# Kernel optimization log

Measured on AMD Instinct MI355X. Metric: run time of the kernel, lower is better.

Reference implementation:

```python
import jax, jax.numpy as jnp
import numpy as np

B, D, N_LAYER = 16384, 1024, 4  # cross_layer=3 -> n_layer=4
BN_EPS = 1e-5


def setup_inputs() -> dict:
    key = jax.random.key(0)
    kx, kw, kb = jax.random.split(key, 3)
    x = jax.random.normal(kx, (B, D), dtype=jnp.float32)
    weight_w = jax.random.normal(kw, (N_LAYER, D), dtype=jnp.float32)
    weight_b = jax.random.normal(kb, (N_LAYER, D), dtype=jnp.float32)
    return {"x": x, "weight_w": weight_w, "weight_b": weight_b}


def reference(x, weight_w, weight_b):
    # Per layer: res = BN(res + x0 * (res . w_l) + b_l)
    # (x0 res^T) @ w == x0 * (res . w): avoids the (B,D,D) outer product.
    x0 = x
    res = x
    for i in range(weight_w.shape[0]):
        s = res @ weight_w[i]                      # (B,) dot per row
        res = res + x0 * s[:, None] + weight_b[i]  # (B,D)
        mu = jnp.mean(res, axis=0)                 # BatchNorm1d, affine=False, train mode
        var = jnp.var(res, axis=0)                 # biased variance
        res = (res - mu) * jax.lax.rsqrt(var + BN_EPS)
    return res
```

## Files before the change

kernel.cpp:

```cpp
#include <hip/hip_runtime.h>


#define BB 16384
#define DD 1024
#define NL 4
#define BN_EPS 1e-5f

constexpr int ABLK = 1024;
constexpr int ROWS_PER_BLK = BB / ABLK;
constexpr int NB1 = 64;
constexpr int RED0 = ABLK / NB1;

template <bool FIRST>
__global__ __launch_bounds__(256) void layer_kernel(
    const float* __restrict__ x0,
    const float* Rin,
    float*       Rout,
    const float* __restrict__ w,
    const float* __restrict__ bias,
    const float* __restrict__ scale,
    const float* __restrict__ shift,
    float* __restrict__ Psum,
    float* __restrict__ Psq)
{
    __shared__ float red[2][2][4];
    const int tid  = threadIdx.x;
    const int lane = tid & 63;
    const int wv   = tid >> 6;
    const int c    = tid << 2;

    const float4 w4 = *(const float4*)(w + c);
    const float4 b4 = *(const float4*)(bias + c);
    float4 sc4, sh4;
    if (FIRST) {
        sc4 = make_float4(1.f, 1.f, 1.f, 1.f);
        sh4 = make_float4(0.f, 0.f, 0.f, 0.f);
    } else {
        sc4 = *(const float4*)(scale + c);
        sh4 = *(const float4*)(shift + c);
    }

    float4 asum = make_float4(0.f, 0.f, 0.f, 0.f);
    float4 asq  = make_float4(0.f, 0.f, 0.f, 0.f);

    const int r0 = blockIdx.x * ROWS_PER_BLK;

    for (int it = 0; it < ROWS_PER_BLK / 2; ++it) {
        const int r = r0 + it * 2;
        const size_t base0 = (size_t)r * DD + c;
        const size_t base1 = base0 + DD;

        float4 v0 = *(const float4*)(Rin + base0);
        float4 v1 = *(const float4*)(Rin + base1);
        float4 xv0, xv1;
        if (!FIRST) {
            xv0 = *(const float4*)(x0 + base0);
            xv1 = *(const float4*)(x0 + base1);
        }

        v0.x = fmaf(v0.x, sc4.x, sh4.x); v0.y = fmaf(v0.y, sc4.y, sh4.y);
        v0.z = fmaf(v0.z, sc4.z, sh4.z); v0.w = fmaf(v0.w, sc4.w, sh4.w);
        v1.x = fmaf(v1.x, sc4.x, sh4.x); v1.y = fmaf(v1.y, sc4.y, sh4.y);
        v1.z = fmaf(v1.z, sc4.z, sh4.z); v1.w = fmaf(v1.w, sc4.w, sh4.w);
        if (FIRST) { xv0 = v0; xv1 = v1; }

        float p0 = v0.x * w4.x + v0.y * w4.y + v0.z * w4.z + v0.w * w4.w;
        float p1 = v1.x * w4.x + v1.y * w4.y + v1.z * w4.z + v1.w * w4.w;

        #pragma unroll
        for (int off = 32; off; off >>= 1) {
            p0 += __shfl_down(p0, off, 64);
            p1 += __shfl_down(p1, off, 64);
        }
        const int slot = it & 1;
        if (lane == 0) { red[slot][0][wv] = p0; red[slot][1][wv] = p1; }
        __syncthreads();
        const float s0 = red[slot][0][0] + red[slot][0][1] +
                         red[slot][0][2] + red[slot][0][3];
        const float s1 = red[slot][1][0] + red[slot][1][1] +
                         red[slot][1][2] + red[slot][1][3];

        float4 n0, n1;
        n0.x = fmaf(xv0.x, s0, v0.x) + b4.x;
        n0.y = fmaf(xv0.y, s0, v0.y) + b4.y;
        n0.z = fmaf(xv0.z, s0, v0.z) + b4.z;
        n0.w = fmaf(xv0.w, s0, v0.w) + b4.w;
        n1.x = fmaf(xv1.x, s1, v1.x) + b4.x;
        n1.y = fmaf(xv1.y, s1, v1.y) + b4.y;
        n1.z = fmaf(xv1.z, s1, v1.z) + b4.z;
        n1.w = fmaf(xv1.w, s1, v1.w) + b4.w;

        *(float4*)(Rout + base0) = n0;
        *(float4*)(Rout + base1) = n1;

        asum.x += n0.x + n1.x; asum.y += n0.y + n1.y;
        asum.z += n0.z + n1.z; asum.w += n0.w + n1.w;
        asq.x = fmaf(n0.x, n0.x, asq.x); asq.x = fmaf(n1.x, n1.x, asq.x);
        asq.y = fmaf(n0.y, n0.y, asq.y); asq.y = fmaf(n1.y, n1.y, asq.y);
        asq.z = fmaf(n0.z, n0.z, asq.z); asq.z = fmaf(n1.z, n1.z, asq.z);
        asq.w = fmaf(n0.w, n0.w, asq.w); asq.w = fmaf(n1.w, n1.w, asq.w);
    }

    *(float4*)(Psum + (size_t)blockIdx.x * DD + c) = asum;
    *(float4*)(Psq  + (size_t)blockIdx.x * DD + c) = asq;
}

__global__ __launch_bounds__(256) void reduce0_kernel(
    const float* __restrict__ Psum, const float* __restrict__ Psq,
    float* __restrict__ Qsum, float* __restrict__ Qsq)
{
    const int c = threadIdx.x << 2;
    const int j = blockIdx.x;
    float4 a = make_float4(0.f, 0.f, 0.f, 0.f);
    float4 q = make_float4(0.f, 0.f, 0.f, 0.f);
    #pragma unroll
    for (int k = 0; k < RED0; ++k) {
        const size_t off = (size_t)(j * RED0 + k) * DD + c;
        const float4 ps = *(const float4*)(Psum + off);
        const float4 pq = *(const float4*)(Psq + off);
        a.x += ps.x; a.y += ps.y; a.z += ps.z; a.w += ps.w;
        q.x += pq.x; q.y += pq.y; q.z += pq.z; q.w += pq.w;
    }
    *(float4*)(Qsum + (size_t)j * DD + c) = a;
    *(float4*)(Qsq  + (size_t)j * DD + c) = q;
}

__global__ __launch_bounds__(256) void stats_kernel(
    const float* __restrict__ Qsum, const float* __restrict__ Qsq,
    float* __restrict__ scale, float* __restrict__ shift)
{
    const int d = blockIdx.x * 256 + threadIdx.x;
    float s = 0.f, q = 0.f;
    #pragma unroll 8
    for (int k = 0; k < NB1; ++k) {
        s += Qsum[k * DD + d];
        q += Qsq[k * DD + d];
    }
    const float mu  = s * (1.0f / BB);
    const float var = q * (1.0f / BB) - mu * mu;
    const float inv = rsqrtf(var + BN_EPS);
    scale[d] = inv;
    shift[d] = -mu * inv;
}

__global__ __launch_bounds__(256) void finalize_kernel(
    float* __restrict__ R,
    const float* __restrict__ scale, const float* __restrict__ shift)
{
    const size_t total = (size_t)BB * DD / 4;
    const size_t stride = (size_t)gridDim.x * blockDim.x;
    for (size_t i = (size_t)blockIdx.x * blockDim.x + threadIdx.x;
         i < total; i += stride) {
        const int c = (int)(i & (DD / 4 - 1)) << 2;
        float4 v = ((const float4*)R)[i];
        const float4 sc = *(const float4*)(scale + c);
        const float4 sh = *(const float4*)(shift + c);
        v.x = fmaf(v.x, sc.x, sh.x);
        v.y = fmaf(v.y, sc.y, sh.y);
        v.z = fmaf(v.z, sc.z, sh.z);
        v.w = fmaf(v.w, sc.w, sh.w);
        ((float4*)R)[i] = v;
    }
}

extern "C" void kernel_launch(void* const* d_in, const int* in_sizes, int n_in,
                              void* d_out, int out_size, void* d_ws, size_t ws_size,
                              hipStream_t stream) {
    const float* x  = (const float*)d_in[0];
    const float* ww = (const float*)d_in[1];
    const float* wb = (const float*)d_in[2];
    float* out = (float*)d_out;
    float* ws  = (float*)d_ws;

    float* Psum  = ws;
    float* Psq   = Psum + (size_t)ABLK * DD;
    float* Qsum  = Psq  + (size_t)ABLK * DD;
    float* Qsq   = Qsum + (size_t)NB1 * DD;
    float* scale = Qsq  + (size_t)NB1 * DD;
    float* shift = scale + DD;

    for (int l = 0; l < NL; ++l) {
        const float* w = ww + (size_t)l * DD;
        const float* b = wb + (size_t)l * DD;
        if (l == 0) {
            layer_kernel<true><<<ABLK, 256, 0, stream>>>(
                x, x, out, w, b, scale, shift, Psum, Psq);
        } else {
            layer_kernel<false><<<ABLK, 256, 0, stream>>>(
                x, out, out, w, b, scale, shift, Psum, Psq);
        }
        reduce0_kernel<<<NB1, 256, 0, stream>>>(Psum, Psq, Qsum, Qsq);
        stats_kernel<<<DD / 256, 256, 0, stream>>>(Qsum, Qsq, scale, shift);
    }
    finalize_kernel<<<2048, 256, 0, stream>>>(out, scale, shift);
}
```

Before: 266.3 us.

## Fuse all cross layers into one cooperative persistent kernel with register-resident rows

Replaces the per-layer kernel sequence (layer, two-stage reduction, stats, finalize) with a single cooperative kernel. Each thread keeps its 32 rows of the residual in registers across layers, and grid-wide syncs compute the BatchNorm statistics. This removes launch overhead and the residual round-trip through global memory each layer. The risks are high register pressure with possible spills, low occupancy of one block per CU, and grid sync latency. The old multi-kernel path remains as a fallback if the cooperative launch fails.

Result: slower. 849.4 us (+219.0%).

```diff
diff --git a/kernel.cpp b/kernel.cpp
--- a/kernel.cpp
+++ b/kernel.cpp
@@ -1,4 +1,7 @@
 #include <hip/hip_runtime.h>
+#include <hip/hip_cooperative_groups.h>
+
+namespace cg = cooperative_groups;
 
 
 #define BB 16384
@@ -6,6 +9,157 @@
 #define NL 4
 #define BN_EPS 1e-5f
 
+constexpr int CGRID = 256;
+constexpr int CTPB  = 512;
+constexpr int CRPB  = BB / CGRID;
+constexpr int CRPT  = CRPB / 2;
+constexpr int GRP   = 8;
+constexpr int NGRP  = CRPT / GRP;
+constexpr int PROWS = CGRID * 2;
+
+__global__ __launch_bounds__(CTPB, 2) void crossnet_coop(
+    const float* __restrict__ x,
+    const float* __restrict__ ww,
+    const float* __restrict__ wb,
+    float* __restrict__ out,
+    float* __restrict__ Psum,
+    float* __restrict__ Psq,
+    float* __restrict__ scale,
+    float* __restrict__ shift)
+{
+    cg::grid_group grid = cg::this_grid();
+    __shared__ float red[2][GRP][8];
+    __shared__ float sA[32][16];
+    __shared__ float sQ[32][16];
+
+    const int t    = threadIdx.x;
+    const int lane = t & 63;
+    const int wv   = t >> 6;
+    const int half = wv >> 2;
+    const int c    = (t & 255) << 2;
+    const int b    = blockIdx.x;
+    const int r0   = b * CRPB + half * CRPT;
+
+    float4 res[CRPT];
+    #pragma unroll
+    for (int r = 0; r < CRPT; ++r)
+        res[r] = *(const float4*)(x + (size_t)(r0 + r) * DD + c);
+
+    float4 sc4 = make_float4(1.f, 1.f, 1.f, 1.f);
+    float4 sh4 = make_float4(0.f, 0.f, 0.f, 0.f);
+
+    for (int l = 0; l < NL; ++l) {
+        const float4 w4 = *(const float4*)(ww + (size_t)l * DD + c);
+        const float4 b4 = *(const float4*)(wb + (size_t)l * DD + c);
+
+        if (l > 0) {
+            #pragma unroll
+            for (int r = 0; r < CRPT; ++r) {
+                res[r].x = fmaf(res[r].x, sc4.x, sh4.x);
+                res[r].y = fmaf(res[r].y, sc4.y, sh4.y);
+                res[r].z = fmaf(res[r].z, sc4.z, sh4.z);
+                res[r].w = fmaf(res[r].w, sc4.w, sh4.w);
+            }
+        }
+
+        float4 asum = make_float4(0.f, 0.f, 0.f, 0.f);
+        float4 asq  = make_float4(0.f, 0.f, 0.f, 0.f);
+
+        for (int g = 0; g < NGRP; ++g) {
+            float4 xg[GRP];
+            if (l > 0) {
+                #pragma unroll
+                for (int j = 0; j < GRP; ++j)
+                    xg[j] = *(const float4*)(x + (size_t)(r0 + g * GRP + j) * DD + c);
+            }
+
+            float p[GRP];
+            #pragma unroll
+            for (int j = 0; j < GRP; ++j) {
+                const float4 v = res[g * GRP + j];
+                p[j] = v.x * w4.x + v.y * w4.y + v.z * w4.z + v.w * w4.w;
+            }
+            #pragma unroll
+            for (int off = 32; off; off >>= 1) {
+                #pragma unroll
+                for (int j = 0; j < GRP; ++j)
+                    p[j] += __shfl_down(p[j], off, 64);
+            }
+            const int slot = g & 1;
+            if (lane == 0) {
+                #pragma unroll
+                for (int j = 0; j < GRP; ++j) red[slot][j][wv] = p[j];
+            }
+            __syncthreads();
+
+            const int w0 = half << 2;
+            #pragma unroll
+            for (int j = 0; j < GRP; ++j) {
+                const float s = red[slot][j][w0] + red[slot][j][w0 + 1] +
+                                red[slot][j][w0 + 2] + red[slot][j][w0 + 3];
+                const float4 v  = res[g * GRP + j];
+                const float4 xv = (l == 0) ? v : xg[j];
+                float4 n;
+                n.x = fmaf(xv.x, s, v.x) + b4.x;
+                n.y = fmaf(xv.y, s, v.y) + b4.y;
+                n.z = fmaf(xv.z, s, v.z) + b4.z;
+                n.w = fmaf(xv.w, s, v.w) + b4.w;
+                res[g * GRP + j] = n;
+                asum.x += n.x; asum.y += n.y; asum.z += n.z; asum.w += n.w;
+                asq.x = fmaf(n.x, n.x, asq.x);
+                asq.y = fmaf(n.y, n.y, asq.y);
+                asq.z = fmaf(n.z, n.z, asq.z);
+                asq.w = fmaf(n.w, n.w, asq.w);
+            }
+        }
+
+        const int prow = (b << 1) + half;
+        *(float4*)(Psum + (size_t)prow * DD + c) = asum;
+        *(float4*)(Psq  + (size_t)prow * DD + c) = asq;
+        __threadfence();
+        grid.sync();
+
+        if (b < 64) {
+            const int cl  = (b << 4) + (t & 15);
+            const int seg = t >> 4;
+            float s = 0.f, q = 0.f;
+            #pragma unroll
+            for (int r = seg * (PROWS / 32); r < (seg + 1) * (PROWS / 32); ++r) {
+                s += Psum[(size_t)r * DD + cl];
+                q += Psq[(size_t)r * DD + cl];
+            }
+            sA[seg][t & 15] = s;
+            sQ[seg][t & 15] = q;
+            __syncthreads();
+            if (t < 16) {
+                float ss = 0.f, qq = 0.f;
+                #pragma unroll
+                for (int k = 0; k < 32; ++k) { ss += sA[k][t]; qq += sQ[k][t]; }
+                const float mu  = ss * (1.0f / BB);
+                const float var = qq * (1.0f / BB) - mu * mu;
+                const float inv = rsqrtf(var + BN_EPS);
+                scale[(b << 4) + t] = inv;
+                shift[(b << 4) + t] = -mu * inv;
+            }
+            __threadfence();
+        }
+        grid.sync();
+
+        sc4 = *(const float4*)(scale + c);
+        sh4 = *(const float4*)(shift + c);
+    }
+
+    #pragma unroll
+    for (int r = 0; r < CRPT; ++r) {
+        float4 v = res[r];
+        v.x = fmaf(v.x, sc4.x, sh4.x);
+        v.y = fmaf(v.y, sc4.y, sh4.y);
+        v.z = fmaf(v.z, sc4.z, sh4.z);
+        v.w = fmaf(v.w, sc4.w, sh4.w);
+        *(float4*)(out + (size_t)(r0 + r) * DD + c) = v;
+    }
+}
+
 constexpr int ABLK = 1024;
 constexpr int ROWS_PER_BLK = BB / ABLK;
 constexpr int NB1 = 64;
@@ -13,15 +167,10 @@
 
 template <bool FIRST>
 __global__ __launch_bounds__(256) void layer_kernel(
-    const float* __restrict__ x0,
-    const float* Rin,
-    float*       Rout,
-    const float* __restrict__ w,
-    const float* __restrict__ bias,
-    const float* __restrict__ scale,
-    const float* __restrict__ shift,
-    float* __restrict__ Psum,
-    float* __restrict__ Psq)
+    const float* __restrict__ x0, const float* Rin, float* Rout,
+    const float* __restrict__ w, const float* __restrict__ bias,
+    const float* __restrict__ scale, const float* __restrict__ shift,
+    float* __restrict__ Psum, float* __restrict__ Psq)
 {
     __shared__ float red[2][2][4];
     const int tid  = threadIdx.x;
@@ -42,14 +191,12 @@
 
     float4 asum = make_float4(0.f, 0.f, 0.f, 0.f);
     float4 asq  = make_float4(0.f, 0.f, 0.f, 0.f);
-
     const int r0 = blockIdx.x * ROWS_PER_BLK;
 
     for (int it = 0; it < ROWS_PER_BLK / 2; ++it) {
         const int r = r0 + it * 2;
         const size_t base0 = (size_t)r * DD + c;
         const size_t base1 = base0 + DD;
-
         float4 v0 = *(const float4*)(Rin + base0);
         float4 v1 = *(const float4*)(Rin + base1);
         float4 xv0, xv1;
@@ -57,7 +204,6 @@
             xv0 = *(const float4*)(x0 + base0);
             xv1 = *(const float4*)(x0 + base1);
         }
-
         v0.x = fmaf(v0.x, sc4.x, sh4.x); v0.y = fmaf(v0.y, sc4.y, sh4.y);
         v0.z = fmaf(v0.z, sc4.z, sh4.z); v0.w = fmaf(v0.w, sc4.w, sh4.w);
         v1.x = fmaf(v1.x, sc4.x, sh4.x); v1.y = fmaf(v1.y, sc4.y, sh4.y);
@@ -66,7 +212,6 @@
 
         float p0 = v0.x * w4.x + v0.y * w4.y + v0.z * w4.z + v0.w * w4.w;
         float p1 = v1.x * w4.x + v1.y * w4.y + v1.z * w4.z + v1.w * w4.w;
-
         #pragma unroll
         for (int off = 32; off; off >>= 1) {
             p0 += __shfl_down(p0, off, 64);
@@ -89,7 +234,6 @@
         n1.y = fmaf(xv1.y, s1, v1.y) + b4.y;
         n1.z = fmaf(xv1.z, s1, v1.z) + b4.z;
         n1.w = fmaf(xv1.w, s1, v1.w) + b4.w;
-
         *(float4*)(Rout + base0) = n0;
         *(float4*)(Rout + base1) = n1;
 
@@ -100,7 +244,6 @@
         asq.z = fmaf(n0.z, n0.z, asq.z); asq.z = fmaf(n1.z, n1.z, asq.z);
         asq.w = fmaf(n0.w, n0.w, asq.w); asq.w = fmaf(n1.w, n1.w, asq.w);
     }
-
     *(float4*)(Psum + (size_t)blockIdx.x * DD + c) = asum;
     *(float4*)(Psq  + (size_t)blockIdx.x * DD + c) = asq;
 }
@@ -179,18 +322,26 @@
     float* scale = Qsq  + (size_t)NB1 * DD;
     float* shift = scale + DD;
 
-    for (int l = 0; l < NL; ++l) {
-        const float* w = ww + (size_t)l * DD;
-        const float* b = wb + (size_t)l * DD;
-        if (l == 0) {
-            layer_kernel<true><<<ABLK, 256, 0, stream>>>(
-                x, x, out, w, b, scale, shift, Psum, Psq);
-        } else {
-            layer_kernel<false><<<ABLK, 256, 0, stream>>>(
-                x, out, out, w, b, scale, shift, Psum, Psq);
-        }
-        reduce0_kernel<<<NB1, 256, 0, stream>>>(Psum, Psq, Qsum, Qsq);
-        stats_kernel<<<DD / 256, 256, 0, stream>>>(Qsum, Qsq, scale, shift);
-    }
-    finalize_kernel<<<2048, 256, 0, stream>>>(out, scale, shift);
-}
+    void* args[] = {(void*)&x, (void*)&ww, (void*)&wb, (void*)&out,
+                    (void*)&Psum, (void*)&Psq, (void*)&scale, (void*)&shift};
+    hipError_t err = hipLaunchCooperativeKernel(
+        (const void*)crossnet_coop, dim3(CGRID), dim3(CTPB), args, 0, stream);
+
+    if (err != hipSuccess) {
+        (void)hipGetLastError();
+        for (int l = 0; l < NL; ++l) {
+            const float* w = ww + (size_t)l * DD;
+            const float* b = wb + (size_t)l * DD;
+            if (l == 0) {
+                layer_kernel<true><<<ABLK, 256, 0, stream>>>(
+                    x, x, out, w, b, scale, shift, Psum, Psq);
+            } else {
+                layer_kernel<false><<<ABLK, 256, 0, stream>>>(
+                    x, out, out, w, b, scale, shift, Psum, Psq);
+            }
+            reduce0_kernel<<<NB1, 256, 0, stream>>>(Psum, Psq, Qsum, Qsq);
+            stats_kernel<<<DD / 256, 256, 0, stream>>>(Qsum, Qsq, scale, shift);
+        }
+        finalize_kernel<<<2048, 256, 0, stream>>>(out, scale, shift);
+    }
+}
```
